# Kernel optimization log

Hardware: AMD Instinct MI355X
Metric: run time of the kernel (lower is better)

## Reference

```python
import jax, jax.numpy as jnp
import numpy as np

D_MODEL = 1024
N_HEADS = 16
HEAD_DIM = D_MODEL // N_HEADS
B, S = 4, 2048


def setup_inputs() -> dict:
    key = jax.random.key(0)
    ks = jax.random.split(key, 12)
    scale = 1.0 / np.sqrt(D_MODEL)
    inp = {
        "query": jax.random.normal(ks[0], (B, S, D_MODEL), dtype=jnp.float32),
        "key": jax.random.normal(ks[1], (B, S, D_MODEL), dtype=jnp.float32),
        "value": jax.random.normal(ks[2], (B, S, D_MODEL), dtype=jnp.float32),
        "mask": jnp.ones((B, 1, S), dtype=jnp.int32),
        "Wq": jax.random.normal(ks[3], (D_MODEL, D_MODEL), dtype=jnp.float32) * scale,
        "bq": jnp.zeros((D_MODEL,), dtype=jnp.float32),
        "Wk": jax.random.normal(ks[4], (D_MODEL, D_MODEL), dtype=jnp.float32) * scale,
        "bk": jnp.zeros((D_MODEL,), dtype=jnp.float32),
        "Wv": jax.random.normal(ks[5], (D_MODEL, D_MODEL), dtype=jnp.float32) * scale,
        "bv": jnp.zeros((D_MODEL,), dtype=jnp.float32),
        "Wo": jax.random.normal(ks[6], (D_MODEL, D_MODEL), dtype=jnp.float32) * scale,
        "bo": jnp.zeros((D_MODEL,), dtype=jnp.float32),
    }
    return inp


def reference(query, key, value, mask, Wq, bq, Wk, bk, Wv, bv, Wo, bo):
    bsz = query.shape[0]
    # Linear projections (torch nn.Linear: x @ W.T + b), split into heads -> [b, h, s, d]
    def proj(x, W, b):
        y = jnp.einsum("bse,de->bsd", x, W) + b
        return y.reshape(bsz, -1, N_HEADS, HEAD_DIM).transpose(0, 2, 1, 3)

    q = proj(query, Wq, bq)
    k = proj(key, Wk, bk)
    v = proj(value, Wv, bv)

    # NOTE: faithful to source — scale by 1/sqrt(d_model), not 1/sqrt(head_dim)
    scores = jnp.einsum("bhqd,bhkd->bhqk", q, k) / jnp.sqrt(jnp.asarray(D_MODEL, q.dtype))
    # mask [b, 1, s_k] -> unsqueeze(1) -> [b, 1, 1, s_k]; fill -inf where mask == 0
    m = mask[:, None, :, :]
    scores = jnp.where(m == 0, jnp.asarray(-jnp.inf, scores.dtype), scores)
    p_attn = jax.nn.softmax(scores, axis=-1)
    ctx = jnp.einsum("bhqk,bhkd->bhqd", p_attn, v)

    concat = ctx.transpose(0, 2, 1, 3).reshape(bsz, -1, D_MODEL)
    out = jnp.einsum("bse,de->bsd", concat, Wo) + bo
    return out
```

## Files before the change

kernel.cpp:

```cpp
#include <hip/hip_runtime.h>
#include <hip/hip_bf16.h>

typedef unsigned short u16;
typedef __attribute__((ext_vector_type(4))) short short4v;
typedef __attribute__((ext_vector_type(8))) short short8;
typedef __attribute__((ext_vector_type(4))) float float4v;

__device__ __forceinline__ void async_copy16(const void* g, void* l) {
  __builtin_amdgcn_global_load_lds(
      (const __attribute__((address_space(1))) unsigned int*)g,
      (__attribute__((address_space(3))) unsigned int*)l,
      16, 0, 0);
}

__device__ __forceinline__ u16 f2bf(float f) {
  __hip_bfloat16 h = __float2bfloat16(f);
  return *reinterpret_cast<u16*>(&h);
}

struct CArgs {
  const float* in[7];
  u16* out[7];
  int n[7];
};

__global__ void conv_bf16(CArgs a) {
  int t = blockIdx.y;
  int n = a.n[t];
  long i = ((long)blockIdx.x * blockDim.x + threadIdx.x) * 8;
  if (i >= n) return;
  const float4v* f = (const float4v*)(a.in[t] + i);
  float4v lo = f[0], hi = f[1];
  u16 o[8];
  o[0] = f2bf(lo.x); o[1] = f2bf(lo.y); o[2] = f2bf(lo.z); o[3] = f2bf(lo.w);
  o[4] = f2bf(hi.x); o[5] = f2bf(hi.y); o[6] = f2bf(hi.z); o[7] = f2bf(hi.w);
  *(short8*)(a.out[t] + i) = *(const short8*)o;
}

template <bool OUT_F32>
__global__ __launch_bounds__(256, 2)
void gemm_bt(const u16* __restrict__ A, const u16* __restrict__ W,
             const float* __restrict__ bias, void* __restrict__ Cp,
             int M, int N, int K, int mode) {
  __shared__ __attribute__((aligned(16))) u16 As[128 * 32];
  __shared__ __attribute__((aligned(16))) u16 Ws[128 * 32];

  const int tid  = threadIdx.x;
  const int lane = tid & 63;
  const int wave = tid >> 6;
  const int ln15 = lane & 15;
  const int quad = lane >> 4;
  const int m0 = blockIdx.y * 128;
  const int n0 = blockIdx.x * 128;
  const int wm = (wave & 1) * 64;
  const int wn = (wave >> 1) * 64;

  float4v acc[4][4];
#pragma unroll
  for (int i = 0; i < 4; i++)
#pragma unroll
    for (int j = 0; j < 4; j++) acc[i][j] = (float4v)0.0f;

  for (int k0 = 0; k0 < K; k0 += 32) {
#pragma unroll
    for (int c = 0; c < 2; c++) {
      int e = (c * 256 + tid) * 8;
      int r = e >> 5, col = e & 31;
      async_copy16(A + (size_t)(m0 + r) * K + k0 + col, (void*)(As + e));
      async_copy16(W + (size_t)(n0 + r) * K + k0 + col, (void*)(Ws + e));
    }
    __syncthreads();

    short8 af[4], bfr[4];
#pragma unroll
    for (int i = 0; i < 4; i++)
      af[i] = *(const short8*)(As + (wm + i * 16 + ln15) * 32 + quad * 8);
#pragma unroll
    for (int j = 0; j < 4; j++)
      bfr[j] = *(const short8*)(Ws + (wn + j * 16 + ln15) * 32 + quad * 8);
#pragma unroll
    for (int i = 0; i < 4; i++)
#pragma unroll
      for (int j = 0; j < 4; j++)
        acc[i][j] = __builtin_amdgcn_mfma_f32_16x16x32_bf16(af[i], bfr[j], acc[i][j], 0, 0, 0);
    __syncthreads();
  }

#pragma unroll
  for (int j = 0; j < 4; j++) {
    int n = n0 + wn + j * 16 + ln15;
    float bval = bias[n];
#pragma unroll
    for (int i = 0; i < 4; i++) {
#pragma unroll
      for (int r = 0; r < 4; r++) {
        int m = m0 + wm + i * 16 + quad * 4 + r;
        float v = acc[i][j][r] + bval;
        size_t addr;
        if (mode == 0) {
          addr = (size_t)m * N + n;
        } else {
          int b = m >> 11, s = m & 2047;
          int h = n >> 6, dh = n & 63;
          if (mode == 1) addr = (((size_t)(b * 16 + h)) * 2048 + s) * 64 + dh;
          else           addr = (((size_t)(b * 16 + h)) * 64 + dh) * 2048 + s;
        }
        if (OUT_F32) ((float*)Cp)[addr] = v;
        else         ((u16*)Cp)[addr] = f2bf(v);
      }
    }
  }
}

#define QP 72
__global__ __launch_bounds__(256, 2)
void attn(const u16* __restrict__ Q, const u16* __restrict__ K,
          const u16* __restrict__ Vt, const int* __restrict__ mask,
          u16* __restrict__ Ct) {
  __shared__ __attribute__((aligned(16))) u16 Qs[128 * QP];
  __shared__ __attribute__((aligned(16))) u16 Ks[2][64 * QP];
  __shared__ __attribute__((aligned(16))) u16 Vs[2][64 * QP];
  __shared__ __attribute__((aligned(16))) u16 Ps[128 * QP];

  const int tid  = threadIdx.x;
  const int lane = tid & 63;
  const int wave = tid >> 6;
  const int ln15 = lane & 15;
  const int quad = lane >> 4;
  const int bh = blockIdx.y;
  const int b = bh >> 4, h = bh & 15;
  const int q0 = blockIdx.x * 128;
  const int qr0 = wave * 32;

  const u16* Qg = Q + ((size_t)bh * 2048 + q0) * 64;
  const u16* Kg = K + (size_t)bh * 2048 * 64;
  const u16* Vg = Vt + (size_t)bh * 64 * 2048;

#pragma unroll
  for (int c = 0; c < 4; c++) {
    int e = (c * 256 + tid) * 8;
    int r = e >> 6, col = e & 63;
    *(short8*)(Qs + r * QP + col) = *(const short8*)(Qg + e);
  }
#pragma unroll
  for (int c = 0; c < 2; c++) {
    int e = (c * 256 + tid) * 8;
    int r = e >> 6, col = e & 63;
    *(short8*)(Ks[0] + r * QP + col) = *(const short8*)(Kg + (size_t)r * 64 + col);
    *(short8*)(Vs[0] + r * QP + col) = *(const short8*)(Vg + (size_t)r * 2048 + col);
  }

  float4v acc_o[2][4];
#pragma unroll
  for (int i = 0; i < 2; i++)
#pragma unroll
    for (int j = 0; j < 4; j++) acc_o[i][j] = (float4v)0.0f;
  float lrow[2][4];
#pragma unroll
  for (int i = 0; i < 2; i++)
#pragma unroll
    for (int r = 0; r < 4; r++) lrow[i][r] = 0.0f;

  for (int t = 0; t < 32; t++) {
    const int buf = t & 1;
    __syncthreads();

    short8 kreg[2], vreg[2];
    const bool havenext = (t + 1) < 32;
    if (havenext) {
      int kt2 = (t + 1) * 64;
#pragma unroll
      for (int c = 0; c < 2; c++) {
        int e = (c * 256 + tid) * 8;
        int r = e >> 6, col = e & 63;
        kreg[c] = *(const short8*)(Kg + (size_t)(kt2 + r) * 64 + col);
        vreg[c] = *(const short8*)(Vg + (size_t)r * 2048 + kt2 + col);
      }
    }

    float4v sacc[2][4];
#pragma unroll
    for (int i = 0; i < 2; i++)
#pragma unroll
      for (int j = 0; j < 4; j++) sacc[i][j] = (float4v)0.0f;
#pragma unroll
    for (int kk = 0; kk < 64; kk += 32) {
      short8 af[2], bfr[4];
#pragma unroll
      for (int i = 0; i < 2; i++)
        af[i] = *(const short8*)(Qs + (qr0 + i * 16 + ln15) * QP + kk + quad * 8);
#pragma unroll
      for (int j = 0; j < 4; j++)
        bfr[j] = *(const short8*)(Ks[buf] + (j * 16 + ln15) * QP + kk + quad * 8);
#pragma unroll
      for (int i = 0; i < 2; i++)
#pragma unroll
        for (int j = 0; j < 4; j++)
          sacc[i][j] = __builtin_amdgcn_mfma_f32_16x16x32_bf16(af[i], bfr[j], sacc[i][j], 0, 0, 0);
    }

    float mb[4];
#pragma unroll
    for (int j = 0; j < 4; j++)
      mb[j] = (mask[b * 2048 + t * 64 + j * 16 + ln15] == 0) ? -1e30f : 0.0f;

#pragma unroll
    for (int i = 0; i < 2; i++) {
#pragma unroll
      for (int r = 0; r < 4; r++) {
        int prow = (qr0 + i * 16 + quad * 4 + r) * QP;
        float sum = 0.0f;
#pragma unroll
        for (int j = 0; j < 4; j++) {
          float p = __expf(sacc[i][j][r] * 0.03125f + mb[j]);
          sum += p;
          Ps[prow + j * 16 + ln15] = f2bf(p);
        }
        lrow[i][r] += sum;
      }
    }

    if (havenext) {
#pragma unroll
      for (int c = 0; c < 2; c++) {
        int e = (c * 256 + tid) * 8;
        int r = e >> 6, col = e & 63;
        *(short8*)(Ks[buf ^ 1] + r * QP + col) = kreg[c];
        *(short8*)(Vs[buf ^ 1] + r * QP + col) = vreg[c];
      }
    }

#pragma unroll
    for (int kk = 0; kk < 64; kk += 32) {
      short8 af[2], bfr[4];
#pragma unroll
      for (int i = 0; i < 2; i++)
        af[i] = *(const short8*)(Ps + (qr0 + i * 16 + ln15) * QP + kk + quad * 8);
#pragma unroll
      for (int jd = 0; jd < 4; jd++)
        bfr[jd] = *(const short8*)(Vs[buf] + (jd * 16 + ln15) * QP + kk + quad * 8);
#pragma unroll
      for (int i = 0; i < 2; i++)
#pragma unroll
        for (int jd = 0; jd < 4; jd++)
          acc_o[i][jd] = __builtin_amdgcn_mfma_f32_16x16x32_bf16(af[i], bfr[jd], acc_o[i][jd], 0, 0, 0);
    }
  }

#pragma unroll
  for (int i = 0; i < 2; i++) {
#pragma unroll
    for (int r = 0; r < 4; r++) {
      float l = lrow[i][r];
      l += __shfl_xor(l, 1);
      l += __shfl_xor(l, 2);
      l += __shfl_xor(l, 4);
      l += __shfl_xor(l, 8);
      float inv = 1.0f / l;
      int s = q0 + qr0 + i * 16 + quad * 4 + r;
#pragma unroll
      for (int jd = 0; jd < 4; jd++) {
        float v = acc_o[i][jd][r] * inv;
        Ct[((size_t)(b * 2048 + s)) * 1024 + h * 64 + jd * 16 + ln15] = f2bf(v);
      }
    }
  }
}


extern "C" void kernel_launch(void* const* d_in, const int* in_sizes, int n_in,
                              void* d_out, int out_size, void* d_ws, size_t ws_size,
                              hipStream_t stream) {
  int iq, ik, iv, im, iWq, ibq, iWk, ibk, iWv, ibv, iWo, ibo;
  if (in_sizes[0] == 8388608) {
    iq = 0; ik = 1; iv = 2; im = 3;
    iWq = 4; ibq = 5; iWk = 6; ibk = 7; iWv = 8; ibv = 9; iWo = 10; ibo = 11;
  } else {
    iWk = 0; iWo = 1; iWq = 2; iWv = 3;
    ibk = 4; ibo = 5; ibq = 6; ibv = 7;
    ik = 8; im = 9; iq = 10; iv = 11;
  }
  const float* query = (const float*)d_in[iq];
  const float* key   = (const float*)d_in[ik];
  const float* value = (const float*)d_in[iv];
  const int*   mask  = (const int*)d_in[im];
  const float* Wq = (const float*)d_in[iWq];
  const float* bq = (const float*)d_in[ibq];
  const float* Wk = (const float*)d_in[iWk];
  const float* bk = (const float*)d_in[ibk];
  const float* Wv = (const float*)d_in[iWv];
  const float* bv = (const float*)d_in[ibv];
  const float* Wo = (const float*)d_in[iWo];
  const float* bo = (const float*)d_in[ibo];

  const long U  = 8388608;
  const long Wn = 1048576;
  u16* ws = (u16*)d_ws;
  u16* cq   = ws;
  u16* ck   = cq + U;
  u16* cv   = ck + U;
  u16* cWq  = cv + U;
  u16* cWk  = cWq + Wn;
  u16* cWv  = cWk + Wn;
  u16* cWo  = cWv + Wn;
  u16* qws  = cWo + Wn;
  u16* kws  = qws + U;
  u16* vtws = cq;
  u16* cws  = ck;

  dim3 blk(256);

  CArgs ca;
  ca.in[0] = query; ca.out[0] = cq;  ca.n[0] = (int)U;
  ca.in[1] = key;   ca.out[1] = ck;  ca.n[1] = (int)U;
  ca.in[2] = value; ca.out[2] = cv;  ca.n[2] = (int)U;
  ca.in[3] = Wq;    ca.out[3] = cWq; ca.n[3] = (int)Wn;
  ca.in[4] = Wk;    ca.out[4] = cWk; ca.n[4] = (int)Wn;
  ca.in[5] = Wv;    ca.out[5] = cWv; ca.n[5] = (int)Wn;
  ca.in[6] = Wo;    ca.out[6] = cWo; ca.n[6] = (int)Wn;
  conv_bf16<<<dim3(4096, 7), blk, 0, stream>>>(ca);

  dim3 gproj(8, 64);
  gemm_bt<false><<<gproj, blk, 0, stream>>>(cq, cWq, bq, qws, 8192, 1024, 1024, 1);
  gemm_bt<false><<<gproj, blk, 0, stream>>>(ck, cWk, bk, kws, 8192, 1024, 1024, 1);
  gemm_bt<false><<<gproj, blk, 0, stream>>>(cv, cWv, bv, vtws, 8192, 1024, 1024, 2);
  attn<<<dim3(16, 64), blk, 0, stream>>>(qws, kws, vtws, mask, cws);
  gemm_bt<true><<<gproj, blk, 0, stream>>>(cws, cWo, bo, d_out, 8192, 1024, 1024, 0);
}
```

Before: 447.4 us.

## Keep Q and P in registers in attention, swizzle K/V LDS, raise occupancy

The attention kernel now holds Q fragments in registers and computes S transposed (K as the A operand), so each lane owns one query row. P stays in registers and is redistributed with cross-lane shuffles into the MFMA B operand, which removes the Ps LDS round trip and the Qs buffer. K/V tiles use an XOR swizzle instead of padding, which shrinks LDS enough to allow launch bounds of 4 blocks per CU. Costs are extra shuffle and select instructions and more register pressure under the tighter bound.

```diff
diff --git a/kernel.cpp b/kernel.cpp
--- a/kernel.cpp
+++ b/kernel.cpp
@@ -16,6 +16,10 @@
 __device__ __forceinline__ u16 f2bf(float f) {
   __hip_bfloat16 h = __float2bfloat16(f);
   return *reinterpret_cast<u16*>(&h);
+}
+
+__device__ __forceinline__ unsigned pack2(float a, float b) {
+  return (unsigned)f2bf(a) | ((unsigned)f2bf(b) << 16);
 }
 
 struct CArgs {
@@ -112,15 +116,13 @@
   }
 }
 
-#define QP 72
-__global__ __launch_bounds__(256, 2)
+#define SWZ(c, r) ((c) ^ (((r) & 7) << 3))
+__global__ __launch_bounds__(256, 4)
 void attn(const u16* __restrict__ Q, const u16* __restrict__ K,
           const u16* __restrict__ Vt, const int* __restrict__ mask,
           u16* __restrict__ Ct) {
-  __shared__ __attribute__((aligned(16))) u16 Qs[128 * QP];
-  __shared__ __attribute__((aligned(16))) u16 Ks[2][64 * QP];
-  __shared__ __attribute__((aligned(16))) u16 Vs[2][64 * QP];
-  __shared__ __attribute__((aligned(16))) u16 Ps[128 * QP];
+  __shared__ __attribute__((aligned(16))) u16 Ks[2][64 * 64];
+  __shared__ __attribute__((aligned(16))) u16 Vs[2][64 * 64];
 
   const int tid  = threadIdx.x;
   const int lane = tid & 63;
@@ -132,34 +134,33 @@
   const int q0 = blockIdx.x * 128;
   const int qr0 = wave * 32;
 
-  const u16* Qg = Q + ((size_t)bh * 2048 + q0) * 64;
+  const u16* Qg = Q + ((size_t)bh * 2048 + q0 + qr0) * 64;
   const u16* Kg = K + (size_t)bh * 2048 * 64;
   const u16* Vg = Vt + (size_t)bh * 64 * 2048;
-
-#pragma unroll
-  for (int c = 0; c < 4; c++) {
-    int e = (c * 256 + tid) * 8;
-    int r = e >> 6, col = e & 63;
-    *(short8*)(Qs + r * QP + col) = *(const short8*)(Qg + e);
-  }
+  const int* mg = mask + b * 2048;
+
+  short8 qf[2][2];
+#pragma unroll
+  for (int i = 0; i < 2; i++)
+#pragma unroll
+    for (int kx = 0; kx < 2; kx++)
+      qf[i][kx] = *(const short8*)(Qg + (size_t)(i * 16 + ln15) * 64 + kx * 32 + quad * 8);
+
 #pragma unroll
   for (int c = 0; c < 2; c++) {
     int e = (c * 256 + tid) * 8;
     int r = e >> 6, col = e & 63;
-    *(short8*)(Ks[0] + r * QP + col) = *(const short8*)(Kg + (size_t)r * 64 + col);
-    *(short8*)(Vs[0] + r * QP + col) = *(const short8*)(Vg + (size_t)r * 2048 + col);
-  }
-
-  float4v acc_o[2][4];
-#pragma unroll
-  for (int i = 0; i < 2; i++)
-#pragma unroll
-    for (int j = 0; j < 4; j++) acc_o[i][j] = (float4v)0.0f;
-  float lrow[2][4];
-#pragma unroll
-  for (int i = 0; i < 2; i++)
-#pragma unroll
-    for (int r = 0; r < 4; r++) lrow[i][r] = 0.0f;
+    int sc = SWZ(col, r);
+    *(short8*)(Ks[0] + r * 64 + sc) = *(const short8*)(Kg + (size_t)r * 64 + col);
+    *(short8*)(Vs[0] + r * 64 + sc) = *(const short8*)(Vg + (size_t)r * 2048 + col);
+  }
+
+  float4v acc[4][2];
+#pragma unroll
+  for (int jd = 0; jd < 4; jd++)
+#pragma unroll
+    for (int i = 0; i < 2; i++) acc[jd][i] = (float4v)0.0f;
+  float lrow[2] = {0.0f, 0.0f};
 
   for (int t = 0; t < 32; t++) {
     const int buf = t & 1;
@@ -178,46 +179,34 @@
       }
     }
 
-    float4v sacc[2][4];
-#pragma unroll
-    for (int i = 0; i < 2; i++)
-#pragma unroll
-      for (int j = 0; j < 4; j++) sacc[i][j] = (float4v)0.0f;
-#pragma unroll
-    for (int kk = 0; kk < 64; kk += 32) {
-      short8 af[2], bfr[4];
-#pragma unroll
-      for (int i = 0; i < 2; i++)
-        af[i] = *(const short8*)(Qs + (qr0 + i * 16 + ln15) * QP + kk + quad * 8);
-#pragma unroll
-      for (int j = 0; j < 4; j++)
-        bfr[j] = *(const short8*)(Ks[buf] + (j * 16 + ln15) * QP + kk + quad * 8);
-#pragma unroll
-      for (int i = 0; i < 2; i++)
-#pragma unroll
-        for (int j = 0; j < 4; j++)
-          sacc[i][j] = __builtin_amdgcn_mfma_f32_16x16x32_bf16(af[i], bfr[j], sacc[i][j], 0, 0, 0);
-    }
-
-    float mb[4];
-#pragma unroll
-    for (int j = 0; j < 4; j++)
-      mb[j] = (mask[b * 2048 + t * 64 + j * 16 + ln15] == 0) ? -1e30f : 0.0f;
-
-#pragma unroll
-    for (int i = 0; i < 2; i++) {
-#pragma unroll
-      for (int r = 0; r < 4; r++) {
-        int prow = (qr0 + i * 16 + quad * 4 + r) * QP;
-        float sum = 0.0f;
-#pragma unroll
-        for (int j = 0; j < 4; j++) {
-          float p = __expf(sacc[i][j][r] * 0.03125f + mb[j]);
-          sum += p;
-          Ps[prow + j * 16 + ln15] = f2bf(p);
-        }
-        lrow[i][r] += sum;
-      }
+    unsigned pk[2][4][2];
+#pragma unroll
+    for (int j = 0; j < 4; j++) {
+      const int krow = j * 16 + ln15;
+      short8 kf0 = *(const short8*)(Ks[buf] + krow * 64 + SWZ(quad * 8, krow));
+      short8 kf1 = *(const short8*)(Ks[buf] + krow * 64 + SWZ(32 + quad * 8, krow));
+      float4v s0 = (float4v)0.0f, s1 = (float4v)0.0f;
+      s0 = __builtin_amdgcn_mfma_f32_16x16x32_bf16(kf0, qf[0][0], s0, 0, 0, 0);
+      s0 = __builtin_amdgcn_mfma_f32_16x16x32_bf16(kf1, qf[0][1], s0, 0, 0, 0);
+      s1 = __builtin_amdgcn_mfma_f32_16x16x32_bf16(kf0, qf[1][0], s1, 0, 0, 0);
+      s1 = __builtin_amdgcn_mfma_f32_16x16x32_bf16(kf1, qf[1][1], s1, 0, 0, 0);
+      int4 m4 = *(const int4*)(mg + t * 64 + j * 16 + quad * 4);
+      float mb0 = (m4.x == 0) ? -1e30f : 0.0f;
+      float mb1 = (m4.y == 0) ? -1e30f : 0.0f;
+      float mb2 = (m4.z == 0) ? -1e30f : 0.0f;
+      float mb3 = (m4.w == 0) ? -1e30f : 0.0f;
+      float p00 = __expf(s0[0] * 0.03125f + mb0);
+      float p01 = __expf(s0[1] * 0.03125f + mb1);
+      float p02 = __expf(s0[2] * 0.03125f + mb2);
+      float p03 = __expf(s0[3] * 0.03125f + mb3);
+      float p10 = __expf(s1[0] * 0.03125f + mb0);
+      float p11 = __expf(s1[1] * 0.03125f + mb1);
+      float p12 = __expf(s1[2] * 0.03125f + mb2);
+      float p13 = __expf(s1[3] * 0.03125f + mb3);
+      lrow[0] += (p00 + p01) + (p02 + p03);
+      lrow[1] += (p10 + p11) + (p12 + p13);
+      pk[0][j][0] = pack2(p00, p01); pk[0][j][1] = pack2(p02, p03);
+      pk[1][j][0] = pack2(p10, p11); pk[1][j][1] = pack2(p12, p13);
     }
 
     if (havenext) {
@@ -225,44 +214,61 @@
       for (int c = 0; c < 2; c++) {
         int e = (c * 256 + tid) * 8;
         int r = e >> 6, col = e & 63;
-        *(short8*)(Ks[buf ^ 1] + r * QP + col) = kreg[c];
-        *(short8*)(Vs[buf ^ 1] + r * QP + col) = vreg[c];
-      }
-    }
-
-#pragma unroll
-    for (int kk = 0; kk < 64; kk += 32) {
-      short8 af[2], bfr[4];
-#pragma unroll
-      for (int i = 0; i < 2; i++)
-        af[i] = *(const short8*)(Ps + (qr0 + i * 16 + ln15) * QP + kk + quad * 8);
-#pragma unroll
-      for (int jd = 0; jd < 4; jd++)
-        bfr[jd] = *(const short8*)(Vs[buf] + (jd * 16 + ln15) * QP + kk + quad * 8);
-#pragma unroll
-      for (int i = 0; i < 2; i++)
-#pragma unroll
-        for (int jd = 0; jd < 4; jd++)
-          acc_o[i][jd] = __builtin_amdgcn_mfma_f32_16x16x32_bf16(af[i], bfr[jd], acc_o[i][jd], 0, 0, 0);
+        int sc = SWZ(col, r);
+        *(short8*)(Ks[buf ^ 1] + r * 64 + sc) = kreg[c];
+        *(short8*)(Vs[buf ^ 1] + r * 64 + sc) = vreg[c];
+      }
+    }
+
+#pragma unroll
+    for (int kx = 0; kx < 2; kx++) {
+      const int j0 = kx * 2, j1 = j0 + 1;
+      short8 bp[2];
+#pragma unroll
+      for (int i = 0; i < 2; i++) {
+        unsigned t16[2], t32[2], t48[2];
+#pragma unroll
+        for (int w = 0; w < 2; w++) {
+          unsigned vlo = (quad < 2) ? pk[i][j0][w] : pk[i][j1][w];
+          unsigned vhi = (quad < 2) ? pk[i][j1][w] : pk[i][j0][w];
+          t16[w] = (unsigned)__shfl_xor((int)vlo, 16);
+          t32[w] = (unsigned)__shfl_xor((int)vhi, 32);
+          t48[w] = (unsigned)__shfl_xor((int)vhi, 48);
+        }
+        union { unsigned w4[4]; short8 s8; } u;
+        u.w4[0] = (quad == 0) ? pk[i][j0][0] : (quad == 1) ? t48[0] : (quad == 2) ? t32[0] : t16[0];
+        u.w4[1] = (quad == 0) ? pk[i][j0][1] : (quad == 1) ? t48[1] : (quad == 2) ? t32[1] : t16[1];
+        u.w4[2] = (quad == 0) ? t16[0] : (quad == 1) ? t32[0] : (quad == 2) ? t48[0] : pk[i][j1][0];
+        u.w4[3] = (quad == 0) ? t16[1] : (quad == 1) ? t32[1] : (quad == 2) ? t48[1] : pk[i][j1][1];
+        bp[i] = u.s8;
+      }
+#pragma unroll
+      for (int jd = 0; jd < 4; jd++) {
+        const int vrow = jd * 16 + ln15;
+        short8 vf = *(const short8*)(Vs[buf] + vrow * 64 + SWZ(kx * 32 + quad * 8, vrow));
+#pragma unroll
+        for (int i = 0; i < 2; i++)
+          acc[jd][i] = __builtin_amdgcn_mfma_f32_16x16x32_bf16(vf, bp[i], acc[jd][i], 0, 0, 0);
+      }
     }
   }
 
 #pragma unroll
   for (int i = 0; i < 2; i++) {
-#pragma unroll
-    for (int r = 0; r < 4; r++) {
-      float l = lrow[i][r];
-      l += __shfl_xor(l, 1);
-      l += __shfl_xor(l, 2);
-      l += __shfl_xor(l, 4);
-      l += __shfl_xor(l, 8);
-      float inv = 1.0f / l;
-      int s = q0 + qr0 + i * 16 + quad * 4 + r;
-#pragma unroll
-      for (int jd = 0; jd < 4; jd++) {
-        float v = acc_o[i][jd][r] * inv;
-        Ct[((size_t)(b * 2048 + s)) * 1024 + h * 64 + jd * 16 + ln15] = f2bf(v);
-      }
+    float l = lrow[i];
+    l += __shfl_xor(l, 16);
+    l += __shfl_xor(l, 32);
+    float inv = 1.0f / l;
+    int s = q0 + qr0 + i * 16 + ln15;
+    u16* base = Ct + ((size_t)(b * 2048 + s)) * 1024 + h * 64 + quad * 4;
+#pragma unroll
+    for (int jd = 0; jd < 4; jd++) {
+      u16 o[4];
+      o[0] = f2bf(acc[jd][i][0] * inv);
+      o[1] = f2bf(acc[jd][i][1] * inv);
+      o[2] = f2bf(acc[jd][i][2] * inv);
+      o[3] = f2bf(acc[jd][i][3] * inv);
+      *(short4v*)(base + jd * 16) = *(const short4v*)o;
     }
   }
 }
```

Result: slower. 580.2 us (+29.7%).
